# Kernel tuning notes

Measured on AMD Instinct MI355X. Metric: run time of the kernel, lower is better.

The kernel has to match this reference:

```python
import jax, jax.numpy as jnp
import numpy as np

B, N, CIN, DIM = 4, 16384, 32, 256
NPOINT, NNEIGH = 2048, 16
BN_EPS = 1e-5


def setup_inputs() -> dict:
    key = jax.random.key(0)
    ks = jax.random.split(key, 6)
    return {
        "xyz": jax.random.normal(ks[0], (B, N, 3), jnp.float32),
        "points": jax.random.normal(ks[1], (B, N, CIN), jnp.float32),
        "fc1_w": jax.random.normal(ks[2], (CIN, DIM), jnp.float32) * 0.05,
        "fc1_b": jnp.zeros((DIM,), jnp.float32),
        "conv1_w": jax.random.normal(ks[3], (DIM, DIM), jnp.float32) * 0.05,
        "conv1_b": jnp.zeros((DIM,), jnp.float32),
        "conv2_w": jax.random.normal(ks[4], (DIM, DIM), jnp.float32) * 0.05,
        "conv2_b": jnp.zeros((DIM,), jnp.float32),
        "bn1_g": jnp.ones((DIM,), jnp.float32),
        "bn1_b": jnp.zeros((DIM,), jnp.float32),
        "bn2_g": jnp.ones((DIM,), jnp.float32),
        "bn2_b": jnp.zeros((DIM,), jnp.float32),
        "bn_g": jnp.ones((DIM,), jnp.float32),
        "bn_b": jnp.zeros((DIM,), jnp.float32),
        "npoint": NPOINT,
        "nneigh": NNEIGH,
    }


def _gather(p, i):
    # p: [B, N, ...], i: [B, ...int] -> per-batch fancy index
    return jax.vmap(lambda a, b: a[b])(p, i)


def _batchnorm(x, g, b):
    # x: [B, S, C]; torch BatchNorm1d training-mode forward over (B, S)
    m = x.mean((0, 1), keepdims=True)
    v = x.var((0, 1), keepdims=True)  # biased variance, as torch uses in forward
    return (x - m) * jax.lax.rsqrt(v + BN_EPS) * g + b


def _fps(xyz, npoint):
    # furthest point sampling, seeded at index 0 (pointnet2_utils convention)
    Bn, Nn, _ = xyz.shape
    dist0 = jnp.full((Bn, Nn), jnp.inf, xyz.dtype)
    far0 = jnp.zeros((Bn,), jnp.int32)

    def step(carry, _):
        dist, far = carry
        cent = _gather(xyz, far)  # [B, 3]
        d = jnp.sum((xyz - cent[:, None, :]) ** 2, axis=-1)  # [B, N]
        dist = jnp.minimum(dist, d)
        nxt = jnp.argmax(dist, axis=-1).astype(jnp.int32)
        return (dist, nxt), far

    _, idx = jax.lax.scan(step, (dist0, far0), None, length=npoint)
    return idx.T  # [B, npoint]


def _square_distance(a, b):
    # a: [B, S, 3], b: [B, N, 3] -> [B, S, N]
    return (jnp.sum(a * a, -1)[..., :, None]
            + jnp.sum(b * b, -1)[..., None, :]
            - 2.0 * jnp.einsum('bsc,bnc->bsn', a, b))


def reference(xyz, points, fc1_w, fc1_b, conv1_w, conv1_b, conv2_w, conv2_b,
              bn1_g, bn1_b, bn2_g, bn2_b, bn_g, bn_b, npoint, nneigh):
    fps_idx = _fps(jax.lax.stop_gradient(xyz), npoint)          # [B, S]
    new_xyz = _gather(xyz, fps_idx)                              # [B, S, 3]

    h = points @ fc1_w + fc1_b                                   # [B, N, D]
    points_ori = _gather(h, fps_idx)                             # [B, S, D]

    t = jax.nn.relu(_batchnorm(h @ conv1_w.T + conv1_b, bn1_g, bn1_b))
    h = h + jax.nn.relu(_batchnorm(t @ conv2_w.T + conv2_b, bn2_g, bn2_b))

    d = _square_distance(jax.lax.stop_gradient(new_xyz), jax.lax.stop_gradient(xyz))
    _, idx = jax.lax.top_k(-d, nneigh)                           # [B, S, K] smallest dists
    grouped = _gather(h, idx)                                    # [B, S, K, D]
    new_points = points_ori + grouped.max(axis=2)                # [B, S, D]
    new_points = _batchnorm(new_points, bn_g, bn_b)
    return new_xyz, new_points
```

## Files before the change

### kernel.cpp

```cpp
#include <hip/hip_runtime.h>
#include <math.h>

#define Bn   4
#define Nn   16384
#define CINn 32
#define DIMn 256
#define Sn   2048
#define KNEI 16
#define BNEPS 1e-5f
#define MROWS (Bn * Nn)
#define SROWS (Bn * Sn)

#define NWORK 248
#define NBLK  (NWORK + Bn)

struct FusedSync {
    unsigned stage[8];
    unsigned prog[Bn];
};

#define UMAX_DPP(v, ctl, rmask)                                               \
    {                                                                         \
        unsigned _o = (unsigned)__builtin_amdgcn_update_dpp(                  \
            0, (int)(v), (ctl), (rmask), 0xf, true);                          \
        (v) = ((v) > _o) ? (v) : _o;                                          \
    }
#define WAVE_UMAX64(v)                                                        \
    UMAX_DPP(v, 0x111, 0xf) UMAX_DPP(v, 0x112, 0xf) UMAX_DPP(v, 0x114, 0xf)  \
    UMAX_DPP(v, 0x118, 0xf) UMAX_DPP(v, 0x142, 0xa) UMAX_DPP(v, 0x143, 0xc)
#define U64MAX_DPP16(khi, klo, ctl)                                           \
    {                                                                         \
        unsigned _lo2 = (unsigned)__builtin_amdgcn_update_dpp(                \
            0, (int)(klo), (ctl), 0xf, 0xf, true);                            \
        unsigned _hi2 = (unsigned)__builtin_amdgcn_update_dpp(                \
            0, (int)(khi), (ctl), 0xf, 0xf, true);                            \
        const bool _g = (_hi2 > (khi)) || (_hi2 == (khi) && _lo2 > (klo));    \
        (khi) = _g ? _hi2 : (khi);                                            \
        (klo) = _g ? _lo2 : (klo);                                            \
    }

__global__ __launch_bounds__(64) void fps_zero_kernel(unsigned* __restrict__ s)
{
    if (threadIdx.x < 12) s[threadIdx.x] = 0u;
}

template <bool BT, bool AFF>
__device__ void gemm_team(const float* A, const float* Bm, const float* bias,
                          const float* asc, const float* ash, float* C,
                          int K, int tile, bool act, float* lAs, float* lBs,
                          int ts)
{
    const int tx = ts & 15;
    const int ty = ts >> 4;
    const int r0 = (tile >> 2) * 64;
    const int c0 = (tile & 3) * 64;
    const int rrA = ts >> 2;
    const int kkA = (ts & 3) * 4;
    float acc[4][4] = {};
    for (int kc = 0; kc < K; kc += 16) {
        if (act) {
            const float4 v = *reinterpret_cast<const float4*>(
                &A[(size_t)(r0 + rrA) * K + kc + kkA]);
            const float vv[4] = {v.x, v.y, v.z, v.w};
#pragma unroll
            for (int m = 0; m < 4; ++m) {
                float xv = vv[m];
                if (AFF) {
                    const int k = kc + kkA + m;
                    xv = fmaxf(fmaf(xv, asc[k], ash[k]), 0.0f);
                }
                lAs[(kkA + m) * 64 + rrA] = xv;
            }
            if (BT) {
                const float4 u = *reinterpret_cast<const float4*>(
                    &Bm[(size_t)(c0 + rrA) * K + kc + kkA]);
                lBs[(kkA + 0) * 64 + rrA] = u.x;
                lBs[(kkA + 1) * 64 + rrA] = u.y;
                lBs[(kkA + 2) * 64 + rrA] = u.z;
                lBs[(kkA + 3) * 64 + rrA] = u.w;
            } else {
                const int kk = ts >> 4;
                const int cc = (ts & 15) * 4;
                const float4 u = *reinterpret_cast<const float4*>(
                    &Bm[(size_t)(kc + kk) * DIMn + c0 + cc]);
                *reinterpret_cast<float4*>(&lBs[kk * 64 + cc]) = u;
            }
        }
        __syncthreads();
        if (act) {
#pragma unroll
            for (int kk = 0; kk < 16; ++kk) {
                const float4 a = *reinterpret_cast<const float4*>(&lAs[kk * 64 + ty * 4]);
                const float4 bv = *reinterpret_cast<const float4*>(&lBs[kk * 64 + tx * 4]);
                const float av[4] = {a.x, a.y, a.z, a.w};
                const float bw[4] = {bv.x, bv.y, bv.z, bv.w};
#pragma unroll
                for (int i = 0; i < 4; ++i)
#pragma unroll
                    for (int j = 0; j < 4; ++j)
                        acc[i][j] = fmaf(av[i], bw[j], acc[i][j]);
            }
        }
        __syncthreads();
    }
    if (act) {
        const int c = c0 + tx * 4;
#pragma unroll
        for (int i = 0; i < 4; ++i) {
            float4 o;
            o.x = acc[i][0] + bias[c + 0];
            o.y = acc[i][1] + bias[c + 1];
            o.z = acc[i][2] + bias[c + 2];
            o.w = acc[i][3] + bias[c + 3];
            *reinterpret_cast<float4*>(&C[(size_t)(r0 + ty * 4 + i) * DIMn + c]) = o;
        }
    }
}

__device__ inline void stage_sync(unsigned* ctr, int t)
{
    __syncthreads();
    if (t == 0) {
        __hip_atomic_fetch_add(ctr, 1u, __ATOMIC_RELEASE, __HIP_MEMORY_SCOPE_AGENT);
        while (__hip_atomic_load(ctr, __ATOMIC_ACQUIRE, __HIP_MEMORY_SCOPE_AGENT)
               < (unsigned)NWORK)
            __builtin_amdgcn_s_sleep(2);
    }
    __syncthreads();
}

__global__ __launch_bounds__(1024, 1) void fused_kernel(
    const float* __restrict__ xyz, const float* __restrict__ points,
    const float* __restrict__ fc1_w, const float* __restrict__ fc1_b,
    const float* __restrict__ conv1_w, const float* __restrict__ conv1_b,
    const float* __restrict__ conv2_w, const float* __restrict__ conv2_b,
    const float* __restrict__ bn1_g, const float* __restrict__ bn1_b,
    const float* __restrict__ bn2_g, const float* __restrict__ bn2_b,
    float* __restrict__ h0, float* __restrict__ A1, float* __restrict__ A2,
    float* __restrict__ pre, int* __restrict__ fidx,
    float* __restrict__ ps, float* __restrict__ pq, float* __restrict__ scv,
    float* __restrict__ newxyz, FusedSync* sync)
{
    __shared__ char smem[81920];
    __shared__ unsigned long long s_aux[33];
    __shared__ int s_nidx[KNEI];
    const int t = threadIdx.x;

    if (blockIdx.x < Bn) {
#pragma clang fp contract(off)
        float* sx = reinterpret_cast<float*>(smem);
        unsigned long long (*s_wk)[16] =
            reinterpret_cast<unsigned long long (*)[16]>(s_aux);
        const int b = blockIdx.x;
        const int w = t >> 6;
        const int lane = t & 63;
        const float* __restrict__ px = xyz + (size_t)b * Nn * 3;
        float y[16], z[16], dist[16];
#pragma unroll
        for (int a = 0; a < 12; ++a) {
            const float4 v = *reinterpret_cast<const float4*>(&px[48 * t + 4 * a]);
            const float e[4] = {v.x, v.y, v.z, v.w};
#pragma unroll
            for (int c = 0; c < 4; ++c) {
                const int flat = 4 * a + c;
                const int j = flat / 3;
                const int comp = flat - 3 * j;
                if (comp == 0) sx[20 * t + j] = e[c];
                else if (comp == 1) y[j] = e[c];
                else z[j] = e[c];
            }
        }
#pragma unroll
        for (int j = 0; j < 16; ++j) {
            dist[j] = __builtin_huge_valf();
            asm volatile("" : "+v"(y[j]));
            asm volatile("" : "+v"(z[j]));
        }
        float cx = px[0], cy = px[1], cz = px[2];
        if (t == 0) {
            fidx[b * Sn] = 0;
            newxyz[(size_t)b * Sn * 3 + 0] = cx;
            newxyz[(size_t)b * Sn * 3 + 1] = cy;
            newxyz[(size_t)b * Sn * 3 + 2] = cz;
        }
        __syncthreads();
        for (int i = 0; i < Sn - 1; ++i) {
            float bd = -1.0f;
#pragma unroll
            for (int a = 0; a < 4; ++a) {
                const float4 q = *reinterpret_cast<const float4*>(&sx[20 * t + 4 * a]);
                const float xv[4] = {q.x, q.y, q.z, q.w};
#pragma unroll
                for (int c = 0; c < 4; ++c) {
                    const int j = 4 * a + c;
                    const float dx = xv[c] - cx;
                    const float dy = y[j] - cy;
                    const float dz = z[j] - cz;
                    const float d = (dx * dx + dy * dy) + dz * dz;
                    const float nd = fminf(dist[j], d);
                    dist[j] = nd;
                    bd = fmaxf(bd, nd);
                }
            }
            unsigned bn = 0;
#pragma unroll
            for (int j = 15; j >= 0; --j)
                if (dist[j] == bd) bn = 0xFFFFFFFFu - (unsigned)(16 * t + j);
            unsigned bdu = __float_as_uint(bd);
            unsigned m = bdu;
            WAVE_UMAX64(m)
            const unsigned bdw = (unsigned)__builtin_amdgcn_readlane((int)m, 63);
            unsigned q2 = (bdu == bdw) ? bn : 0u;
            WAVE_UMAX64(q2)
            const unsigned bnw = (unsigned)__builtin_amdgcn_readlane((int)q2, 63);
            if (lane == 0)
                s_wk[i & 1][w] = ((unsigned long long)bdw << 32) | bnw;
            __syncthreads();
            const unsigned long long kk = (lane < 16) ? s_wk[i & 1][lane] : 0ull;
            unsigned klo = (unsigned)kk;
            unsigned khi = (unsigned)(kk >> 32);
            U64MAX_DPP16(khi, klo, 0x111)
            U64MAX_DPP16(khi, klo, 0x112)
            U64MAX_DPP16(khi, klo, 0x114)
            U64MAX_DPP16(khi, klo, 0x118)
            const unsigned bnf = (unsigned)__builtin_amdgcn_readlane((int)klo, 15);
            const int wu = (int)(0xFFFFFFFFu - bnf);
            cx = px[3 * wu + 0];
            cy = px[3 * wu + 1];
            cz = px[3 * wu + 2];
            if (t == 0) {
                fidx[b * Sn + i + 1] = wu;
                newxyz[(size_t)(b * Sn + i + 1) * 3 + 0] = cx;
                newxyz[(size_t)(b * Sn + i + 1) * 3 + 1] = cy;
                newxyz[(size_t)(b * Sn + i + 1) * 3 + 2] = cz;
                if (((i + 2) & 255) == 0)
                    __hip_atomic_store(&sync->prog[b], (unsigned)(i + 2),
                                       __ATOMIC_RELEASE, __HIP_MEMORY_SCOPE_AGENT);
            }
        }
        return;
    }

    const int wid = blockIdx.x - Bn;
    const int team = t >> 8;
    const int ts = t & 255;
    float* lAs = reinterpret_cast<float*>(smem) + team * 2048;
    float* lBs = lAs + 1024;
    float* sc1 = scv, *sh1 = scv + 256, *sc2 = scv + 512, *sh2 = scv + 768;

    for (int it = 0; it < 5; ++it) {
        const int tile = it * (NWORK * 4) + wid * 4 + team;
        gemm_team<false, false>(points, fc1_w, fc1_b, nullptr, nullptr, h0,
                                CINn, tile, tile < 4096, lAs, lBs, ts);
    }
    stage_sync(&sync->stage[0], t);
    for (int it = 0; it < 5; ++it) {
        const int tile = it * (NWORK * 4) + wid * 4 + team;
        gemm_team<true, false>(h0, conv1_w, conv1_b, nullptr, nullptr, A1,
                               DIMn, tile, tile < 4096, lAs, lBs, ts);
    }
    stage_sync(&sync->stage[1], t);
    for (int sb = wid; sb < 256; sb += NWORK) {
        if (t < DIMn) {
            float s = 0.0f, q = 0.0f;
            const size_t r0 = (size_t)sb * 256;
            for (int r = 0; r < 256; ++r) {
                const float v = A1[(r0 + r) * DIMn + t];
                s += v;
                q = fmaf(v, v, q);
            }
            ps[sb * DIMn + t] = s;
            pq[sb * DIMn + t] = q;
        }
    }
    stage_sync(&sync->stage[2], t);
    if (wid == 0 && t < DIMn) {
        float s = 0.0f, q = 0.0f;
        for (int i = 0; i < 256; ++i) { s += ps[i * DIMn + t]; q += pq[i * DIMn + t]; }
        const float invN = 1.0f / MROWS;
        const float mean = s * invN;
        const float var = q * invN - mean * mean;
        const float r = 1.0f / sqrtf(var + BNEPS);
        const float scale = bn1_g[t] * r;
        sc1[t] = scale;
        sh1[t] = bn1_b[t] - mean * scale;
    }
    stage_sync(&sync->stage[3], t);
    for (int it = 0; it < 5; ++it) {
        const int tile = it * (NWORK * 4) + wid * 4 + team;
        gemm_team<true, true>(A1, conv2_w, conv2_b, sc1, sh1, A2,
                              DIMn, tile, tile < 4096, lAs, lBs, ts);
    }
    stage_sync(&sync->stage[4], t);
    for (int sb = wid; sb < 256; sb += NWORK) {
        if (t < DIMn) {
            float s = 0.0f, q = 0.0f;
            const size_t r0 = (size_t)sb * 256;
            for (int r = 0; r < 256; ++r) {
                const float v = A2[(r0 + r) * DIMn + t];
                s += v;
                q = fmaf(v, v, q);
            }
            ps[sb * DIMn + t] = s;
            pq[sb * DIMn + t] = q;
        }
    }
    stage_sync(&sync->stage[5], t);
    if (wid == 0 && t < DIMn) {
        float s = 0.0f, q = 0.0f;
        for (int i = 0; i < 256; ++i) { s += ps[i * DIMn + t]; q += pq[i * DIMn + t]; }
        const float invN = 1.0f / MROWS;
        const float mean = s * invN;
        const float var = q * invN - mean * mean;
        const float r = 1.0f / sqrtf(var + BNEPS);
        const float scale = bn2_g[t] * r;
        sc2[t] = scale;
        sh2[t] = bn2_b[t] - mean * scale;
    }
    stage_sync(&sync->stage[6], t);
    for (size_t idx = (size_t)wid * 1024 + t; idx < (size_t)MROWS * DIMn / 4;
         idx += (size_t)NWORK * 1024) {
        const int c4 = (int)(idx & 63);
        const float4 hv = reinterpret_cast<const float4*>(h0)[idx];
        float4 av = reinterpret_cast<float4*>(A2)[idx];
        const float4 s4 = reinterpret_cast<const float4*>(sc2)[c4];
        const float4 b4 = reinterpret_cast<const float4*>(sh2)[c4];
        av.x = hv.x + fmaxf(fmaf(av.x, s4.x, b4.x), 0.0f);
        av.y = hv.y + fmaxf(fmaf(av.y, s4.y, b4.y), 0.0f);
        av.z = hv.z + fmaxf(fmaf(av.z, s4.z, b4.z), 0.0f);
        av.w = hv.w + fmaxf(fmaf(av.w, s4.w, b4.w), 0.0f);
        reinterpret_cast<float4*>(A2)[idx] = av;
    }
    stage_sync(&sync->stage[7], t);

    {
#pragma clang fp contract(off)
        unsigned* s_key = reinterpret_cast<unsigned*>(smem);
        const int b = wid & 3;
        const int w = t >> 6;
        const int lane = t & 63;
        const float* px = xyz + (size_t)b * Nn * 3;
        unsigned cprog = 0;
        for (int q = wid; q < SROWS; q += NWORK) {
            const int s = q >> 2;
            if (t == 0 && cprog < (unsigned)(s + 1)) {
                unsigned p;
                do {
                    p = __hip_atomic_load(&sync->prog[b], __ATOMIC_ACQUIRE,
                                          __HIP_MEMORY_SCOPE_AGENT);
                    if (p < (unsigned)(s + 1)) __builtin_amdgcn_s_sleep(8);
                } while (p < (unsigned)(s + 1));
                cprog = p;
            }
            __syncthreads();
            const int bs = b * Sn + s;
            const float qx = newxyz[(size_t)bs * 3 + 0];
            const float qy = newxyz[(size_t)bs * 3 + 1];
            const float qz = newxyz[(size_t)bs * 3 + 2];
            const float qq = (qx * qx + qy * qy) + qz * qz;
            unsigned long long mkey = ~0ull;
#pragma unroll 4
            for (int u = 0; u < 16; ++u) {
                const int n = t + (u << 10);
                const float bx = px[n * 3 + 0];
                const float by = px[n * 3 + 1];
                const float bz = px[n * 3 + 2];
                const float bb2 = (bx * bx + by * by) + bz * bz;
                const float ab = (qx * bx + qy * by) + qz * bz;
                const float d = (qq + bb2) - 2.0f * ab;
                unsigned u32 = __float_as_uint(d);
                u32 = ((int)u32 < 0) ? ~u32 : (u32 | 0x80000000u);
                s_key[n] = u32;
                const unsigned long long k =
                    ((unsigned long long)u32 << 32) | (unsigned)n;
                mkey = (k < mkey) ? k : mkey;
            }
            __syncthreads();
            for (int r = 0; r < KNEI; ++r) {
                unsigned long long k = mkey;
#pragma unroll
                for (int off = 32; off > 0; off >>= 1) {
                    const unsigned long long o = __shfl_xor(k, off);
                    k = (o < k) ? o : k;
                }
                if (lane == 0) s_aux[w] = k;
                __syncthreads();
                if (w == 0) {
                    unsigned long long kk = (lane < 16) ? s_aux[lane] : ~0ull;
#pragma unroll
                    for (int off = 8; off > 0; off >>= 1) {
                        const unsigned long long o = __shfl_xor(kk, off);
                        kk = (o < kk) ? o : kk;
                    }
                    if (lane == 0) {
                        s_aux[32] = kk;
                        s_nidx[r] = (int)(unsigned)(kk & 0xFFFFFFFFull);
                    }
                }
                __syncthreads();
                const unsigned long long wk = s_aux[32];
                if (wk == mkey) {
                    const int wn = (int)(unsigned)(wk & 0xFFFFFFFFull);
                    s_key[wn] = 0xFFFFFFFFu;
                    mkey = ~0ull;
#pragma unroll 4
                    for (int u = 0; u < 16; ++u) {
                        const int n = t + (u << 10);
                        const unsigned long long kk2 =
                            ((unsigned long long)s_key[n] << 32) | (unsigned)n;
                        mkey = (kk2 < mkey) ? kk2 : mkey;
                    }
                }
            }
            __syncthreads();
            if (t < DIMn) {
                const int fid = fidx[bs];
                const float po = h0[((size_t)b * Nn + fid) * DIMn + t];
                float m = -__builtin_huge_valf();
#pragma unroll
                for (int r = 0; r < KNEI; ++r) {
                    const int n = s_nidx[r];
                    m = fmaxf(m, A2[((size_t)b * Nn + n) * DIMn + t]);
                }
                pre[(size_t)bs * DIMn + t] = po + m;
            }
            __syncthreads();
        }
    }
}

__global__ __launch_bounds__(256) void stats_partial(const float* __restrict__ X,
                                                     int rowsPerBlk,
                                                     float* __restrict__ ps,
                                                     float* __restrict__ pq)
{
    const int c = threadIdx.x;
    const size_t r0 = (size_t)blockIdx.x * rowsPerBlk;
    float s = 0.0f, q = 0.0f;
    for (int r = 0; r < rowsPerBlk; ++r) {
        const float v = X[(r0 + r) * DIMn + c];
        s += v;
        q = fmaf(v, v, q);
    }
    ps[blockIdx.x * DIMn + c] = s;
    pq[blockIdx.x * DIMn + c] = q;
}

__global__ __launch_bounds__(256) void bn_finalize(const float* __restrict__ ps,
                                                   const float* __restrict__ pq,
                                                   int nblk, float invN,
                                                   const float* __restrict__ g,
                                                   const float* __restrict__ bb,
                                                   float* __restrict__ sc,
                                                   float* __restrict__ sh)
{
    const int c = threadIdx.x;
    float s = 0.0f, q = 0.0f;
    for (int i = 0; i < nblk; ++i) {
        s += ps[i * DIMn + c];
        q += pq[i * DIMn + c];
    }
    const float mean = s * invN;
    const float var = q * invN - mean * mean;
    const float r = 1.0f / sqrtf(var + BNEPS);
    const float scale = g[c] * r;
    sc[c] = scale;
    sh[c] = bb[c] - mean * scale;
}

__global__ __launch_bounds__(256) void apply_bn_kernel(const float* __restrict__ pre,
                                                       const float* __restrict__ sc,
                                                       const float* __restrict__ sh,
                                                       float* __restrict__ out)
{
    const size_t i = (size_t)blockIdx.x * 256 + threadIdx.x;
    const int c4 = (int)(i & 63);
    const float4 v = reinterpret_cast<const float4*>(pre)[i];
    const float4 s4 = reinterpret_cast<const float4*>(sc)[c4];
    const float4 b4 = reinterpret_cast<const float4*>(sh)[c4];
    float4 o;
    o.x = fmaf(v.x, s4.x, b4.x);
    o.y = fmaf(v.y, s4.y, b4.y);
    o.z = fmaf(v.z, s4.z, b4.z);
    o.w = fmaf(v.w, s4.w, b4.w);
    reinterpret_cast<float4*>(out)[i] = o;
}

extern "C" void kernel_launch(void* const* d_in, const int* in_sizes, int n_in,
                              void* d_out, int out_size, void* d_ws, size_t ws_size,
                              hipStream_t stream)
{
    (void)in_sizes; (void)n_in; (void)out_size; (void)ws_size;
    const float* xyz     = (const float*)d_in[0];
    const float* points  = (const float*)d_in[1];
    const float* fc1_w   = (const float*)d_in[2];
    const float* fc1_b   = (const float*)d_in[3];
    const float* conv1_w = (const float*)d_in[4];
    const float* conv1_b = (const float*)d_in[5];
    const float* conv2_w = (const float*)d_in[6];
    const float* conv2_b = (const float*)d_in[7];
    const float* bn1_g   = (const float*)d_in[8];
    const float* bn1_b   = (const float*)d_in[9];
    const float* bn2_g   = (const float*)d_in[10];
    const float* bn2_b   = (const float*)d_in[11];
    const float* bn_g    = (const float*)d_in[12];
    const float* bn_b    = (const float*)d_in[13];

    float* out = (float*)d_out;
    float* newxyz = out;
    float* outpts = out + (size_t)Bn * Sn * 3;

    char* w = (char*)d_ws;
    float* h0   = (float*)(w);
    float* A1   = (float*)(w + (64ull << 20));
    float* A2   = (float*)(w + (128ull << 20));
    float* pre  = (float*)(w + (192ull << 20));
    int*   fidx = (int*)  (w + (200ull << 20));
    float* ps   = (float*)(w + (201ull << 20));
    float* pq   = ps + 256 * 256;
    float* scv  = pq + 256 * 256;
    float* sc3  = scv + 1024;
    float* sh3  = sc3 + 256;
    FusedSync* sync = (FusedSync*)(w + (203ull << 20));

    fps_zero_kernel<<<1, 64, 0, stream>>>((unsigned*)sync);
    fused_kernel<<<NBLK, 1024, 0, stream>>>(
        xyz, points, fc1_w, fc1_b, conv1_w, conv1_b, conv2_w, conv2_b,
        bn1_g, bn1_b, bn2_g, bn2_b, h0, A1, A2, pre, fidx, ps, pq, scv,
        newxyz, sync);
    stats_partial<<<64, 256, 0, stream>>>(pre, SROWS / 64, ps, pq);
    bn_finalize<<<1, 256, 0, stream>>>(ps, pq, 64, 1.0f / SROWS, bn_g, bn_b, sc3, sh3);
    apply_bn_kernel<<<(SROWS * DIMn / 4) / 256, 256, 0, stream>>>(pre, sc3, sh3, outpts);
}
```

Before: 4.096 ms.

## Store FPS x/y pairs in LDS and strided point assignment

In the furthest-point-sampling blocks, x and y coordinates of all points are now stored interleaved as float2 in a larger shared buffer, while z stays in registers. Points are assigned to threads with a stride of 1024 instead of 16 contiguous points per thread. The next centroid's x/y is read from LDS instead of global memory, shortening the serial per-iteration dependency. Shared memory grows to 128KB, and the index mapping used for tie-breaking changes.

```diff
diff --git a/kernel.cpp b/kernel.cpp
--- a/kernel.cpp
+++ b/kernel.cpp
@@ -141,41 +141,37 @@
     float* __restrict__ ps, float* __restrict__ pq, float* __restrict__ scv,
     float* __restrict__ newxyz, FusedSync* sync)
 {
-    __shared__ char smem[81920];
+    __shared__ __align__(16) char smem[131072];
     __shared__ unsigned long long s_aux[33];
     __shared__ int s_nidx[KNEI];
     const int t = threadIdx.x;
 
     if (blockIdx.x < Bn) {
 #pragma clang fp contract(off)
-        float* sx = reinterpret_cast<float*>(smem);
+        float2* s_xy = reinterpret_cast<float2*>(smem);
         unsigned long long (*s_wk)[16] =
             reinterpret_cast<unsigned long long (*)[16]>(s_aux);
         const int b = blockIdx.x;
         const int w = t >> 6;
         const int lane = t & 63;
         const float* __restrict__ px = xyz + (size_t)b * Nn * 3;
-        float y[16], z[16], dist[16];
-#pragma unroll
-        for (int a = 0; a < 12; ++a) {
-            const float4 v = *reinterpret_cast<const float4*>(&px[48 * t + 4 * a]);
-            const float e[4] = {v.x, v.y, v.z, v.w};
-#pragma unroll
-            for (int c = 0; c < 4; ++c) {
-                const int flat = 4 * a + c;
-                const int j = flat / 3;
-                const int comp = flat - 3 * j;
-                if (comp == 0) sx[20 * t + j] = e[c];
-                else if (comp == 1) y[j] = e[c];
-                else z[j] = e[c];
-            }
-        }
-#pragma unroll
-        for (int j = 0; j < 16; ++j) {
-            dist[j] = __builtin_huge_valf();
-            asm volatile("" : "+v"(y[j]));
-            asm volatile("" : "+v"(z[j]));
-        }
+        float z[16], dist[16];
+#pragma unroll
+        for (int jp = 0; jp < 8; ++jp) {
+            const int u = jp * 1024 + t;
+            const float x0 = px[6 * u + 0];
+            const float y0 = px[6 * u + 1];
+            z[2 * jp + 0]  = px[6 * u + 2];
+            const float x1 = px[6 * u + 3];
+            const float y1 = px[6 * u + 4];
+            z[2 * jp + 1]  = px[6 * u + 5];
+            float4 q; q.x = x0; q.y = y0; q.z = x1; q.w = y1;
+            *reinterpret_cast<float4*>(&s_xy[2 * u]) = q;
+            dist[2 * jp + 0] = __builtin_huge_valf();
+            dist[2 * jp + 1] = __builtin_huge_valf();
+        }
+#pragma unroll
+        for (int s = 0; s < 16; ++s) asm volatile("" : "+v"(z[s]));
         float cx = px[0], cy = px[1], cz = px[2];
         if (t == 0) {
             fidx[b * Sn] = 0;
@@ -187,25 +183,34 @@
         for (int i = 0; i < Sn - 1; ++i) {
             float bd = -1.0f;
 #pragma unroll
-            for (int a = 0; a < 4; ++a) {
-                const float4 q = *reinterpret_cast<const float4*>(&sx[20 * t + 4 * a]);
-                const float xv[4] = {q.x, q.y, q.z, q.w};
-#pragma unroll
-                for (int c = 0; c < 4; ++c) {
-                    const int j = 4 * a + c;
-                    const float dx = xv[c] - cx;
-                    const float dy = y[j] - cy;
-                    const float dz = z[j] - cz;
+            for (int jp = 0; jp < 8; ++jp) {
+                const float4 q =
+                    *reinterpret_cast<const float4*>(&s_xy[2 * (jp * 1024 + t)]);
+                {
+                    const float dx = q.x - cx;
+                    const float dy = q.y - cy;
+                    const float dz = z[2 * jp] - cz;
                     const float d = (dx * dx + dy * dy) + dz * dz;
-                    const float nd = fminf(dist[j], d);
-                    dist[j] = nd;
+                    const float nd = fminf(dist[2 * jp], d);
+                    dist[2 * jp] = nd;
                     bd = fmaxf(bd, nd);
                 }
+                {
+                    const float dx = q.z - cx;
+                    const float dy = q.w - cy;
+                    const float dz = z[2 * jp + 1] - cz;
+                    const float d = (dx * dx + dy * dy) + dz * dz;
+                    const float nd = fminf(dist[2 * jp + 1], d);
+                    dist[2 * jp + 1] = nd;
+                    bd = fmaxf(bd, nd);
+                }
             }
             unsigned bn = 0;
 #pragma unroll
-            for (int j = 15; j >= 0; --j)
-                if (dist[j] == bd) bn = 0xFFFFFFFFu - (unsigned)(16 * t + j);
+            for (int s = 15; s >= 0; --s)
+                if (dist[s] == bd)
+                    bn = 0xFFFFFFFFu -
+                         (unsigned)(2 * ((s >> 1) * 1024 + t) + (s & 1));
             unsigned bdu = __float_as_uint(bd);
             unsigned m = bdu;
             WAVE_UMAX64(m)
@@ -225,8 +230,9 @@
             U64MAX_DPP16(khi, klo, 0x118)
             const unsigned bnf = (unsigned)__builtin_amdgcn_readlane((int)klo, 15);
             const int wu = (int)(0xFFFFFFFFu - bnf);
-            cx = px[3 * wu + 0];
-            cy = px[3 * wu + 1];
+            const float2 cxy = s_xy[wu];
+            cx = cxy.x;
+            cy = cxy.y;
             cz = px[3 * wu + 2];
             if (t == 0) {
                 fidx[b * Sn + i + 1] = wu;
```

Result: no change. 4.120 ms (median of 2 runs) (+0.6%).
